# Kernel tuning notes

Measured on AMD Instinct MI355X. Metric: run time of the kernel, lower is better.

Reference implementation:

```python
import jax, jax.numpy as jnp
import numpy as np

GAMMA = 1.0
MAX_SIMILARITY = 1.0


def setup_inputs() -> dict:
    key = jax.random.key(0)
    k1, k2, k3 = jax.random.split(key, 3)
    B, Ns, D = 64, 1024, 256
    d_vectors = jax.random.normal(k1, (B, Ns, D), dtype=jnp.float32)
    S = jax.random.uniform(k2, (Ns, Ns), dtype=jnp.float32)  # MinMax-normalized sims in [0,1]
    W = (jax.random.uniform(k3, (Ns, Ns)) > 0.3).astype(jnp.float32)  # binary mask (simmat > 0)
    return {"d_vectors": d_vectors, "S": S, "W": W}


def reference(d_vectors, S, W):
    B, Ns, D = d_vectors.shape
    eye = jnp.eye(Ns, dtype=d_vectors.dtype)
    # pairwise L2 distances via ||a-b||^2 = |a|^2 + |b|^2 - 2 a.b  (batched GEMM)
    sq = jnp.sum(d_vectors * d_vectors, axis=-1)                     # [B, Ns]
    G = jnp.einsum('bnd,bmd->bnm', d_vectors, d_vectors)             # [B, Ns, Ns]
    dist2 = jnp.maximum(sq[:, :, None] + sq[:, None, :] - 2.0 * G, 0.0)
    # diagonal of Kd is zeroed below; offset it so sqrt is safe (output unchanged)
    dist = jnp.sqrt(dist2 + eye[None])
    Kd = jnp.exp(-GAMMA * dist)                                      # gram matrix [B, Ns, Ns]
    Kd_tilde = Kd * (1.0 - eye)                                      # Kd - Kd*I
    S_tilde = S - MAX_SIMILARITY * eye                               # [Ns, Ns]
    diff = W[None] * (Kd_tilde - S_tilde[None])
    numer = jnp.sqrt(jnp.sum(diff * diff, axis=(1, 2)))              # per-batch Frobenius norm
    denom = jnp.sqrt(jnp.sum((W - eye) ** 2))
    return jnp.sum(2.0 * numer / denom)
```

## Files before the change

### kernel.cpp

```cpp
#include <hip/hip_runtime.h>
#include <hip/hip_bf16.h>

#define NB 64
#define NS 1024
#define DD 256
#define NT 36
#define THR 120.0f

typedef __attribute__((ext_vector_type(4))) float f32x4;
typedef __attribute__((ext_vector_type(8))) short bf16x8;
typedef unsigned long long u64;

__device__ __forceinline__ unsigned short f2bf(float x) {
  union { float f; unsigned int u; } c; c.f = x;
  unsigned int r = c.u + 0x7fffu + ((c.u >> 16) & 1u);
  return (unsigned short)(r >> 16);
}

__device__ __forceinline__ unsigned int pk_fp8x4(float x, float y, float z, float w) {
  unsigned int v = 0;
#if __has_builtin(__builtin_amdgcn_cvt_pk_fp8_f32)
  v = __builtin_amdgcn_cvt_pk_fp8_f32(x, y, v, false);
  v = __builtin_amdgcn_cvt_pk_fp8_f32(z, w, v, true);
#else
  asm("v_cvt_pk_fp8_f32 %0, %1, %2" : "+v"(v) : "v"(x), "v"(y));
  asm("v_cvt_pk_fp8_f32 %0, %1, %2 op_sel:[0,0,1]" : "+v"(v) : "v"(z), "v"(w));
#endif
  return v;
}


__global__ __launch_bounds__(128) void prep_kernel(const float* __restrict__ din,
                                                   unsigned char* __restrict__ dbf3,
                                                   float* __restrict__ sq,
                                                   int write_bf) {
  __shared__ unsigned char T[16][256];
  const int px = (int)blockIdx.x;
  const int wid = (int)threadIdx.x >> 6;
  const int l = (int)threadIdx.x & 63;
  const int tb = (px & 7) * 512 + (px >> 3);
  const int b = tb >> 6, rt = tb & 63;
  const float4* src =
      reinterpret_cast<const float4*>(din + ((size_t)b * NS + rt * 16) * DD) + l;
  #pragma unroll
  for (int j = 0; j < 8; ++j) {
    const int ri = wid * 8 + j;
    float4 v = src[ri * 64];
    float s = v.x * v.x + v.y * v.y + v.z * v.z + v.w * v.w;
    #pragma unroll
    for (int off = 32; off > 0; off >>= 1) s += __shfl_xor(s, off, 64);
    if (l == 0) sq[(size_t)b * NS + rt * 16 + ri] = s;
    if (write_bf) {
      const unsigned int w4 = pk_fp8x4(v.x, v.y, v.z, v.w);
      const int gp = l ^ ((ri & 15) << 2);
      *reinterpret_cast<unsigned int*>(&T[ri][gp * 4]) = w4;
    }
  }
  if (!write_bf) return;
  __syncthreads();
  unsigned char* dst = dbf3 + (((size_t)b * 8) * 64 + rt) * 512 + (size_t)l * 8;
  #pragma unroll
  for (int q = 0; q < 4; ++q) {
    const int kg = wid * 4 + q;
    const int gd = kg * 8 + (l >> 4) * 2;
    const int gp = gd ^ ((l & 15) << 2);
    const u64 frag = *reinterpret_cast<const u64*>(&T[l & 15][gp * 4]);
    *reinterpret_cast<u64*>(dst + (size_t)kg * 64 * 512) = frag;
  }
}

template <int MODE>
__global__ __launch_bounds__(256, 2) void main_kernel(
    const float* __restrict__ dvec, const unsigned char* __restrict__ dbf3,
    const float* __restrict__ sq, const float* __restrict__ S,
    const float* __restrict__ W, float* __restrict__ npart,
    float* __restrict__ dpart, float* __restrict__ cpart) {
  const int tid = threadIdx.x;
  const int lane = tid & 63;
  const int wid = tid >> 6;
  const int orig = (int)blockIdx.x;

  if (orig >= NT * NB) {
    const int blk = orig - NT * NB;
    const int base = blk * 256 + tid;
    float dsum = 0.f, csum = 0.f;
    #pragma unroll
    for (int rpt = 0; rpt < 2; ++rpt) {
      const int idx = base + rpt * 131072;
      float4 w = reinterpret_cast<const float4*>(W)[idx];
      float4 s4 = reinterpret_cast<const float4*>(S)[idx];
      const int e0 = idx << 2;
      const int r = e0 >> 10, c0 = e0 & 1023;
      float wv[4] = {w.x, w.y, w.z, w.w};
      float sv[4] = {s4.x, s4.y, s4.z, s4.w};
      #pragma unroll
      for (int i = 0; i < 4; ++i) {
        const bool dg = (c0 + i) == r;
        const float a = wv[i] - (dg ? 1.0f : 0.0f);
        dsum = fmaf(a, a, dsum);
        const float bq = dg ? (1.0f - sv[i]) : sv[i];
        csum = fmaf(wv[i] * bq, bq, csum);
      }
    }
    #pragma unroll
    for (int off = 32; off > 0; off >>= 1) {
      dsum += __shfl_xor(dsum, off, 64);
      csum += __shfl_xor(csum, off, 64);
    }
    __shared__ float redD[4], redC[4];
    if (lane == 0) { redD[wid] = dsum; redC[wid] = csum; }
    __syncthreads();
    if (tid == 0) {
      dpart[blk] = redD[0] + redD[1] + redD[2] + redD[3];
      cpart[blk] = redC[0] + redC[1] + redC[2] + redC[3];
    }
    return;
  }

  const int wr = wid >> 1;
  const int wc = wid & 1;
  const int bid = (orig & 7) * (NT * NB / 8) + (orig >> 3);
  const int t = bid % NT;
  const int b = bid / NT;
  int u = t, ti = 0;
  while (u >= 8 - ti) { u -= 8 - ti; ++ti; }
  const int tj = ti + u;
  const int brow = ti * 128;
  const int bcol = tj * 128;

  const int rtA0 = ti * 8 + wr * 4;
  const int rtB0 = tj * 8 + wc * 4;

  f32x4 acc[4][4];
  #pragma unroll
  for (int m = 0; m < 4; ++m)
    #pragma unroll
    for (int n = 0; n < 4; ++n) acc[m][n] = f32x4{0.f, 0.f, 0.f, 0.f};

  if (MODE == 0) {
    const unsigned char* pa =
        dbf3 + (((size_t)b * 8) * 64 + rtA0) * 512 + (size_t)lane * 8;
    const unsigned char* pb =
        dbf3 + (((size_t)b * 8) * 64 + rtB0) * 512 + (size_t)lane * 8;
    u64 af[4], bf[4], nf[4];
    #pragma unroll
    for (int m = 0; m < 4; ++m)
      af[m] = *reinterpret_cast<const u64*>(pa + m * 512);
    #pragma unroll
    for (int n = 0; n < 4; ++n)
      bf[n] = *reinterpret_cast<const u64*>(pb + n * 512);
    #pragma unroll
    for (int kg = 0; kg < 8; ++kg) {
      if (kg < 7) {
        #pragma unroll
        for (int m = 0; m < 4; ++m)
          nf[m] = *reinterpret_cast<const u64*>(pa + 32768 + m * 512);
      }
      #pragma unroll
      for (int n = 0; n < 4; ++n) {
        #pragma unroll
        for (int m = 0; m < 4; ++m)
          acc[m][n] = __builtin_amdgcn_mfma_f32_16x16x32_fp8_fp8(
              (long)af[m], (long)bf[n], acc[m][n], 0, 0, 0);
        if (kg < 7)
          bf[n] = *reinterpret_cast<const u64*>(pb + 32768 + n * 512);
      }
      if (kg < 7) {
        #pragma unroll
        for (int m = 0; m < 4; ++m) af[m] = nf[m];
        pa += 32768; pb += 32768;
      }
    }
  } else {
    const float* pbase = dvec + (size_t)b * NS * DD + (lane >> 4) * 8;
    #pragma unroll
    for (int kg = 0; kg < 8; ++kg) {
      bf16x8 af[4], bf[4];
      #pragma unroll
      for (int m = 0; m < 4; ++m) {
        const float* p = pbase + (size_t)((rtA0 + m) * 16 + (lane & 15)) * DD + kg * 32;
        float4 v0 = reinterpret_cast<const float4*>(p)[0];
        float4 v1 = reinterpret_cast<const float4*>(p)[1];
        af[m][0] = (short)f2bf(v0.x); af[m][1] = (short)f2bf(v0.y);
        af[m][2] = (short)f2bf(v0.z); af[m][3] = (short)f2bf(v0.w);
        af[m][4] = (short)f2bf(v1.x); af[m][5] = (short)f2bf(v1.y);
        af[m][6] = (short)f2bf(v1.z); af[m][7] = (short)f2bf(v1.w);
      }
      #pragma unroll
      for (int n = 0; n < 4; ++n) {
        const float* p = pbase + (size_t)((rtB0 + n) * 16 + (lane & 15)) * DD + kg * 32;
        float4 v0 = reinterpret_cast<const float4*>(p)[0];
        float4 v1 = reinterpret_cast<const float4*>(p)[1];
        bf[n][0] = (short)f2bf(v0.x); bf[n][1] = (short)f2bf(v0.y);
        bf[n][2] = (short)f2bf(v0.z); bf[n][3] = (short)f2bf(v0.w);
        bf[n][4] = (short)f2bf(v1.x); bf[n][5] = (short)f2bf(v1.y);
        bf[n][6] = (short)f2bf(v1.z); bf[n][7] = (short)f2bf(v1.w);
      }
      #pragma unroll
      for (int m = 0; m < 4; ++m)
        #pragma unroll
        for (int n = 0; n < 4; ++n)
          acc[m][n] = __builtin_amdgcn_mfma_f32_16x16x32_bf16(af[m], bf[n], acc[m][n], 0, 0, 0);
    }
  }

  const float* sqb = sq + (size_t)b * NS;
  const int hi = lane >> 4, lo = lane & 15;
  float sqc[4];
  #pragma unroll
  for (int n = 0; n < 4; ++n) sqc[n] = sqb[bcol + wc * 64 + n * 16 + lo];
  float dmin = 1e30f;
  #pragma unroll
  for (int m = 0; m < 4; ++m) {
    #pragma unroll
    for (int j = 0; j < 4; ++j) {
      const int r = brow + wr * 64 + m * 16 + hi * 4 + j;
      const float sqr = sqb[r];
      #pragma unroll
      for (int n = 0; n < 4; ++n) {
        const int c = bcol + wc * 64 + n * 16 + lo;
        const float d2 = fmaxf(sqr + sqc[n] - 2.0f * acc[m][n][j], 0.0f);
        dmin = fminf(dmin, (r < c) ? d2 : 1e30f);
      }
    }
  }
  float wsum = 0.f;
  if (__any(dmin < THR)) {
    float lsum = 0.f;
    #pragma unroll
    for (int m = 0; m < 4; ++m) {
      #pragma unroll
      for (int j = 0; j < 4; ++j) {
        const int r = brow + wr * 64 + m * 16 + hi * 4 + j;
        const float sqr = sqb[r];
        #pragma unroll
        for (int n = 0; n < 4; ++n) {
          const int c = bcol + wc * 64 + n * 16 + lo;
          const float d2 = fmaxf(sqr + sqc[n] - 2.0f * acc[m][n][j], 0.0f);
          if ((r < c) && (d2 < THR)) {
            const float kd = __expf(-sqrtf(d2));
            const float wrc = W[(size_t)r * NS + c];
            const float wcr = W[(size_t)c * NS + r];
            const float src_ = S[(size_t)r * NS + c];
            const float scr = S[(size_t)c * NS + r];
            lsum = fmaf(kd, kd * (wrc + wcr) - 2.0f * fmaf(wrc, src_, wcr * scr), lsum);
          }
        }
      }
    }
    #pragma unroll
    for (int off = 32; off > 0; off >>= 1) lsum += __shfl_xor(lsum, off, 64);
    wsum = lsum;
  }
  if (lane == 0) npart[(size_t)bid * 4 + wid] = wsum;
}

__global__ void final_kernel(const float* __restrict__ npart,
                             const float* __restrict__ dpart,
                             const float* __restrict__ cpart,
                             float* __restrict__ out) {
  const int lane = threadIdx.x;
  float dsum = 0.f, csum = 0.f;
  #pragma unroll
  for (int j = 0; j < 8; ++j) {
    dsum += dpart[lane + 64 * j];
    csum += cpart[lane + 64 * j];
  }
  #pragma unroll
  for (int off = 32; off > 0; off >>= 1) {
    dsum += __shfl_xor(dsum, off, 64);
    csum += __shfl_xor(csum, off, 64);
  }
  float nb = 0.f;
  const f32x4* np = reinterpret_cast<const f32x4*>(npart + (size_t)lane * 144);
  #pragma unroll
  for (int j = 0; j < 36; ++j) {
    f32x4 v = np[j];
    nb += v[0] + v[1] + v[2] + v[3];
  }
  float v = 2.0f * sqrtf(csum + nb);
  #pragma unroll
  for (int off = 32; off > 0; off >>= 1) v += __shfl_xor(v, off, 64);
  if (lane == 0) out[0] = v / sqrtf(dsum);
}

extern "C" void kernel_launch(void* const* d_in, const int* in_sizes, int n_in,
                              void* d_out, int out_size, void* d_ws, size_t ws_size,
                              hipStream_t stream) {
  const float* dvec = (const float*)d_in[0];
  const float* S = (const float*)d_in[1];
  const float* W = (const float*)d_in[2];
  float* out = (float*)d_out;

  const size_t bf_bytes = (size_t)NB * NS * DD;
  const size_t sq_bytes = (size_t)NB * NS * sizeof(float);
  const size_t small_bytes = sq_bytes + (9216 + 512 + 512) * sizeof(float);
  const bool full = ws_size >= bf_bytes + small_bytes;

  unsigned char* dbf3;
  float* sqp;
  if (full) {
    dbf3 = (unsigned char*)d_ws;
    sqp = (float*)((char*)d_ws + bf_bytes);
  } else {
    dbf3 = nullptr;
    sqp = (float*)d_ws;
  }
  float* npart = sqp + (size_t)NB * NS;
  float* dpart = npart + 9216;
  float* cpart = dpart + 512;

  prep_kernel<<<4096, 128, 0, stream>>>(dvec, dbf3, sqp, full ? 1 : 0);
  if (full)
    main_kernel<0><<<NT * NB + 512, 256, 0, stream>>>(dvec, dbf3, sqp, S, W,
                                                      npart, dpart, cpart);
  else
    main_kernel<1><<<NT * NB + 512, 256, 0, stream>>>(dvec, dbf3, sqp, S, W,
                                                      npart, dpart, cpart);
  final_kernel<<<1, 64, 0, stream>>>(npart, dpart, cpart, out);
}
```

Before: 42.12 us.

## Use 16x16x128 scaled FP8 MFMA with matching 32-byte fragment layout

Replaces the eight-step K loop of 16x16x32 FP8 MFMAs with two steps of the gfx950 scaled 16x16x128 f8f6f4 MFMA, using unit scales (exponent 127). The prep kernel now writes each lane's fragment as 32 contiguous bytes per 128-wide K chunk, so the main kernel issues wider 32-byte loads. This cuts the MFMA instruction count and the load count, but the explicit software prefetch across K steps is gone and register pressure from the 256-bit operands rises.

```diff
diff --git a/kernel.cpp b/kernel.cpp
--- a/kernel.cpp
+++ b/kernel.cpp
@@ -9,6 +9,8 @@
 
 typedef __attribute__((ext_vector_type(4))) float f32x4;
 typedef __attribute__((ext_vector_type(8))) short bf16x8;
+typedef __attribute__((ext_vector_type(8))) int i32x8;
+typedef __attribute__((ext_vector_type(4))) unsigned int u32x4;
 typedef unsigned long long u64;
 
 __device__ __forceinline__ unsigned short f2bf(float x) {
@@ -31,7 +33,7 @@
 
 
 __global__ __launch_bounds__(128) void prep_kernel(const float* __restrict__ din,
-                                                   unsigned char* __restrict__ dbf3,
+                                                   unsigned char* __restrict__ dbf4,
                                                    float* __restrict__ sq,
                                                    int write_bf) {
   __shared__ unsigned char T[16][256];
@@ -58,20 +60,20 @@
   }
   if (!write_bf) return;
   __syncthreads();
-  unsigned char* dst = dbf3 + (((size_t)b * 8) * 64 + rt) * 512 + (size_t)l * 8;
-  #pragma unroll
-  for (int q = 0; q < 4; ++q) {
-    const int kg = wid * 4 + q;
-    const int gd = kg * 8 + (l >> 4) * 2;
-    const int gp = gd ^ ((l & 15) << 2);
-    const u64 frag = *reinterpret_cast<const u64*>(&T[l & 15][gp * 4]);
-    *reinterpret_cast<u64*>(dst + (size_t)kg * 64 * 512) = frag;
-  }
+  const int kc = wid;
+  const int row = l & 15, cxor = row << 2;
+  const int g0 = kc * 32 + (l >> 4) * 8;
+  const u32x4 lo = *reinterpret_cast<const u32x4*>(&T[row][((g0 + 0) ^ cxor) * 4]);
+  const u32x4 hi = *reinterpret_cast<const u32x4*>(&T[row][((g0 + 4) ^ cxor) * 4]);
+  unsigned char* dst =
+      dbf4 + (((size_t)b * 2 + kc) * 64 + rt) * 2048 + (size_t)l * 32;
+  *reinterpret_cast<u32x4*>(dst) = lo;
+  *reinterpret_cast<u32x4*>(dst + 16) = hi;
 }
 
 template <int MODE>
 __global__ __launch_bounds__(256, 2) void main_kernel(
-    const float* __restrict__ dvec, const unsigned char* __restrict__ dbf3,
+    const float* __restrict__ dvec, const unsigned char* __restrict__ dbf4,
     const float* __restrict__ sq, const float* __restrict__ S,
     const float* __restrict__ W, float* __restrict__ npart,
     float* __restrict__ dpart, float* __restrict__ cpart) {
@@ -139,37 +141,24 @@
 
   if (MODE == 0) {
     const unsigned char* pa =
-        dbf3 + (((size_t)b * 8) * 64 + rtA0) * 512 + (size_t)lane * 8;
+        dbf4 + (((size_t)b * 2) * 64 + rtA0) * 2048 + (size_t)lane * 32;
     const unsigned char* pb =
-        dbf3 + (((size_t)b * 8) * 64 + rtB0) * 512 + (size_t)lane * 8;
-    u64 af[4], bf[4], nf[4];
-    #pragma unroll
-    for (int m = 0; m < 4; ++m)
-      af[m] = *reinterpret_cast<const u64*>(pa + m * 512);
-    #pragma unroll
-    for (int n = 0; n < 4; ++n)
-      bf[n] = *reinterpret_cast<const u64*>(pb + n * 512);
-    #pragma unroll
-    for (int kg = 0; kg < 8; ++kg) {
-      if (kg < 7) {
+        dbf4 + (((size_t)b * 2) * 64 + rtB0) * 2048 + (size_t)lane * 32;
+    #pragma unroll
+    for (int kc = 0; kc < 2; ++kc) {
+      i32x8 av[4], bv[4];
+      #pragma unroll
+      for (int m = 0; m < 4; ++m)
+        av[m] = *reinterpret_cast<const i32x8*>(pa + (size_t)kc * 131072 + m * 2048);
+      #pragma unroll
+      for (int n = 0; n < 4; ++n)
+        bv[n] = *reinterpret_cast<const i32x8*>(pb + (size_t)kc * 131072 + n * 2048);
+      #pragma unroll
+      for (int m = 0; m < 4; ++m)
         #pragma unroll
-        for (int m = 0; m < 4; ++m)
-          nf[m] = *reinterpret_cast<const u64*>(pa + 32768 + m * 512);
-      }
-      #pragma unroll
-      for (int n = 0; n < 4; ++n) {
-        #pragma unroll
-        for (int m = 0; m < 4; ++m)
-          acc[m][n] = __builtin_amdgcn_mfma_f32_16x16x32_fp8_fp8(
-              (long)af[m], (long)bf[n], acc[m][n], 0, 0, 0);
-        if (kg < 7)
-          bf[n] = *reinterpret_cast<const u64*>(pb + 32768 + n * 512);
-      }
-      if (kg < 7) {
-        #pragma unroll
-        for (int m = 0; m < 4; ++m) af[m] = nf[m];
-        pa += 32768; pb += 32768;
-      }
+        for (int n = 0; n < 4; ++n)
+          acc[m][n] = __builtin_amdgcn_mfma_scale_f32_16x16x128_f8f6f4(
+              av[m], bv[n], acc[m][n], 0, 0, 0, 127, 0, 127);
     }
   } else {
     const float* pbase = dvec + (size_t)b * NS * DD + (lane >> 4) * 8;
@@ -297,25 +286,25 @@
   const size_t small_bytes = sq_bytes + (9216 + 512 + 512) * sizeof(float);
   const bool full = ws_size >= bf_bytes + small_bytes;
 
-  unsigned char* dbf3;
+  unsigned char* dbf4;
   float* sqp;
   if (full) {
-    dbf3 = (unsigned char*)d_ws;
+    dbf4 = (unsigned char*)d_ws;
     sqp = (float*)((char*)d_ws + bf_bytes);
   } else {
-    dbf3 = nullptr;
+    dbf4 = nullptr;
     sqp = (float*)d_ws;
   }
   float* npart = sqp + (size_t)NB * NS;
   float* dpart = npart + 9216;
   float* cpart = dpart + 512;
 
-  prep_kernel<<<4096, 128, 0, stream>>>(dvec, dbf3, sqp, full ? 1 : 0);
+  prep_kernel<<<4096, 128, 0, stream>>>(dvec, dbf4, sqp, full ? 1 : 0);
   if (full)
-    main_kernel<0><<<NT * NB + 512, 256, 0, stream>>>(dvec, dbf3, sqp, S, W,
+    main_kernel<0><<<NT * NB + 512, 256, 0, stream>>>(dvec, dbf4, sqp, S, W,
                                                       npart, dpart, cpart);
   else
-    main_kernel<1><<<NT * NB + 512, 256, 0, stream>>>(dvec, dbf3, sqp, S, W,
+    main_kernel<1><<<NT * NB + 512, 256, 0, stream>>>(dvec, dbf4, sqp, S, W,
                                                       npart, dpart, cpart);
   final_kernel<<<1, 64, 0, stream>>>(npart, dpart, cpart, out);
 }
```

Result: faster. 40.13 us (-4.7%).
